# Performance work log

Measured on AMD Instinct MI355X. Metric: run time of the kernel, lower is better.

## Reference

```python
import jax, jax.numpy as jnp
import numpy as np

# ---- static module config (HashEncoder defaults) ----
INPUT_DIM = 3
NUM_LEVELS = 16
LEVEL_DIM = 2
PER_LEVEL_SCALE = 2.0
BASE_RES = 16
LOG2_HASHMAP = 19
MAX_PARAMS = 2 ** LOG2_HASHMAP
S = np.log2(PER_LEVEL_SCALE)  # log2 of per-level scale, as in the CUDA kernel
B_POINTS = 1048576

# per-level table offsets, exactly as in HashEncoder.__init__
_offs = [0]
_off = 0
for _i in range(NUM_LEVELS):
    _res = int(np.ceil(BASE_RES * PER_LEVEL_SCALE ** _i))
    _p = min(MAX_PARAMS, (_res + 1) ** INPUT_DIM)
    _p = int(_p / 8) * 8
    _off += _p
    _offs.append(_off)
OFFSETS = np.array(_offs, dtype=np.int64)
N_ENTRIES = _off  # 7132272

# spatial hash primes from torch-ngp fast_hash (first 3 dims)
PRIMES = np.array([1, 2654435761, 805459861], dtype=np.uint32)


def _encode_level(inputs, emb_level, level, hashmap_size):
    """One resolution level: hash 8 corners, gather, trilinear-interp. inputs: [B,3] in [0,1]."""
    scale = np.float32(np.exp2(level * S) * BASE_RES - 1.0)
    resolution = int(np.ceil(scale)) + 1
    pos = inputs * scale + 0.5
    pos_grid = jnp.floor(pos)
    frac = pos - pos_grid                    # [B,3] trilinear fractions
    pg = pos_grid.astype(jnp.uint32)         # [B,3] base corner
    # kernel hashes whenever the dense grid would exceed the (rounded) table size
    use_hash = (resolution + 1) ** INPUT_DIM > hashmap_size
    hs = np.uint32(hashmap_size)
    out = jnp.zeros((inputs.shape[0], LEVEL_DIM), dtype=inputs.dtype)
    for c in range(2 ** INPUT_DIM):          # 8 corners
        bits = np.array([(c >> d) & 1 for d in range(INPUT_DIM)], dtype=np.uint32)
        w = jnp.prod(jnp.where(bits.astype(bool), frac, 1.0 - frac), axis=-1)  # [B]
        corner = pg + bits                   # [B,3] uint32
        if use_hash:
            h = corner * PRIMES              # uint32 wrap-around multiply
            idx = h[:, 0] ^ h[:, 1] ^ h[:, 2]
        else:
            stride = np.uint32(resolution + 1)
            idx = corner[:, 0] + corner[:, 1] * stride + corner[:, 2] * (stride * stride)
        idx = (idx % hs).astype(jnp.int32)
        out = out + w[:, None] * emb_level[idx]  # irregular gather [B,C]
    return out


def setup_inputs() -> dict:
    key = jax.random.key(0)
    k1, k2 = jax.random.split(key)
    xyz = jax.random.uniform(k1, (B_POINTS, INPUT_DIM), dtype=jnp.float32)
    # reset_parameters: uniform(-1e-4, 1e-4)
    embeddings = jax.random.uniform(k2, (N_ENTRIES, LEVEL_DIM), dtype=jnp.float32,
                                    minval=-1e-4, maxval=1e-4)
    return {"xyz": xyz, "embeddings": embeddings, "normalize": 0}


def reference(xyz, embeddings, normalize):
    # normalize == 0 -> use raw coords (kernel expects [0,1]^3), matching normalize=False path
    inputs = xyz.reshape(-1, INPUT_DIM)
    outs = []
    for l in range(NUM_LEVELS):
        o0, o1 = int(OFFSETS[l]), int(OFFSETS[l + 1])
        outs.append(_encode_level(inputs, embeddings[o0:o1], l, o1 - o0))
    # equivalent to outputs.permute(1,0,2).reshape(B, L*C)
    return jnp.concatenate(outs, axis=-1)
```

## Files before the change

### kernel.cpp

```cpp
#include <hip/hip_runtime.h>

#define NLEVELS 16
#define BLOCK 256
#define PPT 2

struct HashParams {
    unsigned offs[NLEVELS + 1];
    unsigned hsize[NLEVELS];
    unsigned hash_bits;
    unsigned pow2_bits;
};

__global__ void __launch_bounds__(BLOCK)
hashenc_pass1(const float* __restrict__ xyz,
              const float* __restrict__ emb,
              float2* __restrict__ ws,
              HashParams p, int np, int bpl_shift)
{
    const int l = blockIdx.x >> bpl_shift;
    const int chunk = blockIdx.x & ((1 << bpl_shift) - 1);
    const int tid = threadIdx.x;

    const unsigned hs = p.hsize[l];
    const float2* __restrict__ tab = (const float2*)emb + p.offs[l];
    const float scale = (float)((16u << l) - 1u);
    const bool do_hash = (p.hash_bits >> l) & 1u;
    const bool is_pow2 = (p.pow2_bits >> l) & 1u;

    const int base = chunk * (BLOCK * PPT) + tid;

#pragma unroll
    for (int s = 0; s < PPT; ++s) {
        const int pidx = base + s * BLOCK;
        const float x = xyz[pidx * 3 + 0];
        const float y = xyz[pidx * 3 + 1];
        const float z = xyz[pidx * 3 + 2];

        const float px = x * scale + 0.5f;
        const float py = y * scale + 0.5f;
        const float pz = z * scale + 0.5f;
        const float gx = floorf(px), gy = floorf(py), gz = floorf(pz);
        const float fx = px - gx, fy = py - gy, fz = pz - gz;
        const unsigned ix = (unsigned)gx, iy = (unsigned)gy, iz = (unsigned)gz;

        const float wxv[2] = {1.0f - fx, fx};
        const float wyv[2] = {1.0f - fy, fy};
        const float wzv[2] = {1.0f - fz, fz};
        float o0 = 0.0f, o1 = 0.0f;

        if (do_hash && is_pow2) {
            const unsigned m = hs - 1u;
            const unsigned hy0 = iy * 2654435761u;
            const unsigned hz0 = iz * 805459861u;
            const unsigned hy1 = hy0 + 2654435761u;
            const unsigned hz1 = hz0 + 805459861u;
            const unsigned hyz[4] = { hy0 ^ hz0, hy1 ^ hz0, hy0 ^ hz1, hy1 ^ hz1 };

            if (!(ix & 1u)) {
                float4 pr[4];
                unsigned vv[4];
#pragma unroll
                for (int q = 0; q < 4; ++q) {
                    vv[q] = (ix ^ hyz[q]) & m;
                    pr[q] = *reinterpret_cast<const float4*>(tab + (vv[q] & ~1u));
                }
#pragma unroll
                for (int q = 0; q < 4; ++q) {
                    const bool sw = (vv[q] & 1u) != 0u;
                    const float ex0x = sw ? pr[q].z : pr[q].x;
                    const float ex0y = sw ? pr[q].w : pr[q].y;
                    const float ex1x = sw ? pr[q].x : pr[q].z;
                    const float ex1y = sw ? pr[q].y : pr[q].w;
                    const float w0 = wxv[0] * wyv[q & 1] * wzv[(q >> 1) & 1];
                    const float w1 = wxv[1] * wyv[q & 1] * wzv[(q >> 1) & 1];
                    o0 = fmaf(w0, ex0x, o0); o1 = fmaf(w0, ex0y, o1);
                    o0 = fmaf(w1, ex1x, o0); o1 = fmaf(w1, ex1y, o1);
                }
            } else {
                float2 e0[4], e1[4];
#pragma unroll
                for (int q = 0; q < 4; ++q) {
                    e0[q] = tab[(ix ^ hyz[q]) & m];
                    e1[q] = tab[((ix + 1u) ^ hyz[q]) & m];
                }
#pragma unroll
                for (int q = 0; q < 4; ++q) {
                    const float w0 = wxv[0] * wyv[q & 1] * wzv[(q >> 1) & 1];
                    const float w1 = wxv[1] * wyv[q & 1] * wzv[(q >> 1) & 1];
                    o0 = fmaf(w0, e0[q].x, o0); o1 = fmaf(w0, e0[q].y, o1);
                    o0 = fmaf(w1, e1[q].x, o0); o1 = fmaf(w1, e1[q].y, o1);
                }
            }
        } else {
            unsigned idx[8];
            if (do_hash) {
                const unsigned hy0 = iy * 2654435761u;
                const unsigned hz0 = iz * 805459861u;
                const unsigned hy1 = hy0 + 2654435761u;
                const unsigned hz1 = hz0 + 805459861u;
#pragma unroll
                for (int c = 0; c < 8; ++c)
                    idx[c] = ((ix + (c & 1)) ^ ((c & 2) ? hy1 : hy0) ^ ((c & 4) ? hz1 : hz0)) % hs;
            } else {
                const unsigned stride = (16u << l) + 1u;
#pragma unroll
                for (int c = 0; c < 8; ++c) {
                    const unsigned lin = (ix + (c & 1))
                                       + (iy + ((c >> 1) & 1)) * stride
                                       + (iz + ((c >> 2) & 1)) * stride * stride;
                    idx[c] = lin % hs;
                }
            }
            float2 e[8];
#pragma unroll
            for (int c = 0; c < 8; ++c) e[c] = tab[idx[c]];
#pragma unroll
            for (int c = 0; c < 8; ++c) {
                const float w = wxv[c & 1] * wyv[(c >> 1) & 1] * wzv[(c >> 2) & 1];
                o0 = fmaf(w, e[c].x, o0);
                o1 = fmaf(w, e[c].y, o1);
            }
        }

        ws[((size_t)(pidx >> 8) * NLEVELS + l) * 256 + (pidx & 255)] = make_float2(o0, o1);
    }
}

__global__ void __launch_bounds__(BLOCK)
hashenc_pass2(const float2* __restrict__ ws, float* __restrict__ out, int np)
{
    __shared__ float lds[BLOCK * 33];
    const int tid = threadIdx.x;
    const float2* __restrict__ chunk = ws + (size_t)blockIdx.x * (NLEVELS * 256);

#pragma unroll
    for (int l = 0; l < NLEVELS; ++l) {
        const float2 v = chunk[l * 256 + tid];
        lds[tid * 33 + 2 * l + 0] = v.x;
        lds[tid * 33 + 2 * l + 1] = v.y;
    }
    __syncthreads();
    float* __restrict__ ochunk = out + (size_t)blockIdx.x * (BLOCK * 32);
#pragma unroll
    for (int k = 0; k < 32; ++k) {
        const int flat = k * BLOCK + tid;
        const float v = lds[(flat >> 5) * 33 + (flat & 31)];
        __builtin_nontemporal_store(v, ochunk + flat);
    }
}

__global__ void __launch_bounds__(BLOCK)
hashenc_fwd(const float* __restrict__ xyz,
            const float* __restrict__ emb,
            float* __restrict__ out,
            HashParams p)
{
    const int tid = threadIdx.x;
    const long b = (long)blockIdx.x * BLOCK + tid;
    __shared__ float lds[BLOCK * 33];

    const float x = xyz[b * 3 + 0];
    const float y = xyz[b * 3 + 1];
    const float z = xyz[b * 3 + 2];

#pragma unroll
    for (int l = 0; l < NLEVELS; ++l) {
        const float scale = (float)((16u << l) - 1u);
        const float px = x * scale + 0.5f;
        const float py = y * scale + 0.5f;
        const float pz = z * scale + 0.5f;
        const float gx = floorf(px), gy = floorf(py), gz = floorf(pz);
        const float fx = px - gx, fy = py - gy, fz = pz - gz;
        const unsigned ix = (unsigned)gx, iy = (unsigned)gy, iz = (unsigned)gz;
        const unsigned hs = p.hsize[l];
        const float2* __restrict__ tab = (const float2*)emb + p.offs[l];

        unsigned idx[8];
        if ((p.hash_bits >> l) & 1u) {
            const unsigned hy0 = iy * 2654435761u;
            const unsigned hz0 = iz * 805459861u;
            const unsigned hy1 = hy0 + 2654435761u;
            const unsigned hz1 = hz0 + 805459861u;
            if ((p.pow2_bits >> l) & 1u) {
                const unsigned m = hs - 1u;
#pragma unroll
                for (int c = 0; c < 8; ++c)
                    idx[c] = ((ix + (c & 1)) ^ ((c & 2) ? hy1 : hy0) ^ ((c & 4) ? hz1 : hz0)) & m;
            } else {
#pragma unroll
                for (int c = 0; c < 8; ++c)
                    idx[c] = ((ix + (c & 1)) ^ ((c & 2) ? hy1 : hy0) ^ ((c & 4) ? hz1 : hz0)) % hs;
            }
        } else {
            const unsigned stride = (16u << l) + 1u;
#pragma unroll
            for (int c = 0; c < 8; ++c) {
                const unsigned lin = (ix + (c & 1))
                                   + (iy + ((c >> 1) & 1)) * stride
                                   + (iz + ((c >> 2) & 1)) * stride * stride;
                idx[c] = lin % hs;
            }
        }

        float2 e[8];
#pragma unroll
        for (int c = 0; c < 8; ++c) e[c] = tab[idx[c]];

        const float wx[2] = {1.0f - fx, fx};
        const float wy[2] = {1.0f - fy, fy};
        const float wz[2] = {1.0f - fz, fz};
        float o0 = 0.0f, o1 = 0.0f;
#pragma unroll
        for (int c = 0; c < 8; ++c) {
            const float w = wx[c & 1] * wy[(c >> 1) & 1] * wz[(c >> 2) & 1];
            o0 = fmaf(w, e[c].x, o0);
            o1 = fmaf(w, e[c].y, o1);
        }
        lds[tid * 33 + l * 2 + 0] = o0;
        lds[tid * 33 + l * 2 + 1] = o1;
    }

    __syncthreads();
    float* __restrict__ ochunk = out + (long)blockIdx.x * (BLOCK * 32);
#pragma unroll
    for (int k = 0; k < 32; ++k) {
        const int flat = k * BLOCK + tid;
        const float v = lds[(flat >> 5) * 33 + (flat & 31)];
        __builtin_nontemporal_store(v, ochunk + flat);
    }
}

extern "C" void kernel_launch(void* const* d_in, const int* in_sizes, int n_in,
                              void* d_out, int out_size, void* d_ws, size_t ws_size,
                              hipStream_t stream) {
    const float* xyz = (const float*)d_in[0];
    const float* emb = (const float*)d_in[1];
    float* out = (float*)d_out;
    const int B = in_sizes[0] / 3;

    HashParams p;
    p.offs[0] = 0;
    unsigned hash_bits = 0, pow2_bits = 0;
    long off = 0;
    for (int i = 0; i < NLEVELS; ++i) {
        const long res = 16L << i;
        const long dense = (res + 1) * (res + 1) * (res + 1);
        long t = dense < (1L << 19) ? dense : (1L << 19);
        t = (t / 8) * 8;
        p.hsize[i] = (unsigned)t;
        off += t;
        p.offs[i + 1] = (unsigned)off;
        if (dense > t) hash_bits |= (1u << i);
        if ((t & (t - 1)) == 0) pow2_bits |= (1u << i);
    }
    p.hash_bits = hash_bits;
    p.pow2_bits = pow2_bits;

    const size_t need = (size_t)B * NLEVELS * sizeof(float2);
    if (ws_size >= need && (B % (BLOCK * PPT)) == 0 && (B % 256) == 0) {
        int bpl_shift = 0;
        while ((1 << bpl_shift) * (BLOCK * PPT) < B) ++bpl_shift;
        const int bpl = 1 << bpl_shift;
        hashenc_pass1<<<dim3(NLEVELS * bpl), dim3(BLOCK), 0, stream>>>(
            xyz, emb, (float2*)d_ws, p, B, bpl_shift);
        hashenc_pass2<<<dim3(B / 256), dim3(BLOCK), 0, stream>>>(
            (const float2*)d_ws, out, B);
    } else {
        hashenc_fwd<<<dim3(B / BLOCK), dim3(BLOCK), 0, stream>>>(xyz, emb, out, p);
    }
}
```

Before: 572.5 us.

## Stage xyz in LDS and switch workspace to level-major layout with float4 pass2

Pass1 now loads each block's xyz chunk into shared memory with coalesced float4 reads instead of strided scalar loads, and writes its results to a level-major workspace (one contiguous array per level). Pass2 drops the LDS transpose: each thread reads two levels' float2 values and writes one float4 of the output directly. The aim is to cut uncoalesced loads and transpose overhead. In exchange, pass2 reads come from two strided level planes, the nontemporal stores are gone, and pass1 gains a barrier.

New measurement: 584.1 us. 1.02x slower.

```diff
diff --git a/kernel.cpp b/kernel.cpp
--- a/kernel.cpp
+++ b/kernel.cpp
@@ -21,20 +21,31 @@
     const int chunk = blockIdx.x & ((1 << bpl_shift) - 1);
     const int tid = threadIdx.x;
 
+    __shared__ float sxyz[BLOCK * PPT * 3];
+    {
+        const float4* __restrict__ src =
+            (const float4*)(xyz + (size_t)chunk * (BLOCK * PPT) * 3);
+        float4* __restrict__ dst = (float4*)sxyz;
+#pragma unroll
+        for (int i = tid; i < (BLOCK * PPT * 3) / 4; i += BLOCK)
+            dst[i] = src[i];
+    }
+    __syncthreads();
+
     const unsigned hs = p.hsize[l];
     const float2* __restrict__ tab = (const float2*)emb + p.offs[l];
     const float scale = (float)((16u << l) - 1u);
     const bool do_hash = (p.hash_bits >> l) & 1u;
     const bool is_pow2 = (p.pow2_bits >> l) & 1u;
-
-    const int base = chunk * (BLOCK * PPT) + tid;
+    float2* __restrict__ wl = ws + (size_t)l * np;
 
 #pragma unroll
     for (int s = 0; s < PPT; ++s) {
-        const int pidx = base + s * BLOCK;
-        const float x = xyz[pidx * 3 + 0];
-        const float y = xyz[pidx * 3 + 1];
-        const float z = xyz[pidx * 3 + 2];
+        const int lp = s * BLOCK + tid;
+        const int pidx = chunk * (BLOCK * PPT) + lp;
+        const float x = sxyz[lp * 3 + 0];
+        const float y = sxyz[lp * 3 + 1];
+        const float z = sxyz[lp * 3 + 2];
 
         const float px = x * scale + 0.5f;
         const float py = y * scale + 0.5f;
@@ -122,31 +133,19 @@
             }
         }
 
-        ws[((size_t)(pidx >> 8) * NLEVELS + l) * 256 + (pidx & 255)] = make_float2(o0, o1);
+        wl[pidx] = make_float2(o0, o1);
     }
 }
 
 __global__ void __launch_bounds__(BLOCK)
-hashenc_pass2(const float2* __restrict__ ws, float* __restrict__ out, int np)
+hashenc_pass2(const float2* __restrict__ ws, float4* __restrict__ out4, int np)
 {
-    __shared__ float lds[BLOCK * 33];
-    const int tid = threadIdx.x;
-    const float2* __restrict__ chunk = ws + (size_t)blockIdx.x * (NLEVELS * 256);
-
-#pragma unroll
-    for (int l = 0; l < NLEVELS; ++l) {
-        const float2 v = chunk[l * 256 + tid];
-        lds[tid * 33 + 2 * l + 0] = v.x;
-        lds[tid * 33 + 2 * l + 1] = v.y;
-    }
-    __syncthreads();
-    float* __restrict__ ochunk = out + (size_t)blockIdx.x * (BLOCK * 32);
-#pragma unroll
-    for (int k = 0; k < 32; ++k) {
-        const int flat = k * BLOCK + tid;
-        const float v = lds[(flat >> 5) * 33 + (flat & 31)];
-        __builtin_nontemporal_store(v, ochunk + flat);
-    }
+    const int f = blockIdx.x * BLOCK + threadIdx.x;
+    const int p = f >> 3;
+    const int j = f & 7;
+    const float2 a = ws[(size_t)(2 * j) * np + p];
+    const float2 b = ws[(size_t)(2 * j + 1) * np + p];
+    out4[f] = make_float4(a.x, a.y, b.x, b.y);
 }
 
 __global__ void __launch_bounds__(BLOCK)
@@ -257,14 +256,15 @@
     p.pow2_bits = pow2_bits;
 
     const size_t need = (size_t)B * NLEVELS * sizeof(float2);
-    if (ws_size >= need && (B % (BLOCK * PPT)) == 0 && (B % 256) == 0) {
+    const long nf4 = (long)B * 8;
+    if (ws_size >= need && (B % (BLOCK * PPT)) == 0 && (nf4 % BLOCK) == 0) {
         int bpl_shift = 0;
         while ((1 << bpl_shift) * (BLOCK * PPT) < B) ++bpl_shift;
         const int bpl = 1 << bpl_shift;
         hashenc_pass1<<<dim3(NLEVELS * bpl), dim3(BLOCK), 0, stream>>>(
             xyz, emb, (float2*)d_ws, p, B, bpl_shift);
-        hashenc_pass2<<<dim3(B / 256), dim3(BLOCK), 0, stream>>>(
-            (const float2*)d_ws, out, B);
+        hashenc_pass2<<<dim3((int)(nf4 / BLOCK)), dim3(BLOCK), 0, stream>>>(
+            (const float2*)d_ws, (float4*)out, B);
     } else {
         hashenc_fwd<<<dim3(B / BLOCK), dim3(BLOCK), 0, stream>>>(xyz, emb, out, p);
     }
```
